# Kernel optimization log

Hardware: AMD Instinct MI355X
Metric: run time of the kernel (lower is better)

Reference implementation:

```python
import jax, jax.numpy as jnp
import numpy as np

HIDDEN = 1024
HEADS = 16
KNN = 20
EDGE_DICT = 64


def setup_inputs() -> dict:
    key = jax.random.key(0)
    ks = jax.random.split(key, 16)
    B, S, L = 2, 2000, 100
    w = lambda k, shp: jax.random.normal(k, shp, dtype=jnp.float32) * 0.02
    return {
        "c_mask": jax.random.randint(ks[0], (L,), 0, 2),
        "degrees_vec": jax.random.randint(ks[1], (L,), 0, EDGE_DICT),
        "q": jax.random.normal(ks[2], (B, S, HIDDEN), dtype=jnp.float32),
        "k": jax.random.normal(ks[3], (B, S, HIDDEN), dtype=jnp.float32),
        "v": jax.random.normal(ks[4], (B, S, HIDDEN), dtype=jnp.float32),
        "Wq": w(ks[5], (HIDDEN, HIDDEN)), "bq": jnp.zeros((HIDDEN,), jnp.float32),
        "Wk": w(ks[6], (HIDDEN, HIDDEN)), "bk": jnp.zeros((HIDDEN,), jnp.float32),
        "Wv": w(ks[7], (HIDDEN, HIDDEN)), "bv": jnp.zeros((HIDDEN,), jnp.float32),
        "Wo": w(ks[8], (HIDDEN, HIDDEN)), "bo": jnp.zeros((HIDDEN,), jnp.float32),
        "edge_emb": w(ks[9], (EDGE_DICT, HIDDEN)),
        "mask_emb": w(ks[10], (2, HIDDEN)),
    }


def reference(c_mask, degrees_vec, q, k, v, Wq, bq, Wk, bk, Wv, bv, Wo, bo, edge_emb, mask_emb):
    B, S, _ = q.shape
    d = HIDDEN // HEADS
    scale = d ** -0.5
    # torch Linear: x @ W.T + b
    qh = (q @ Wq.T + bq).reshape(B, S, HEADS, d)
    kh = (k @ Wk.T + bk).reshape(B, S, HEADS, d)
    vh = (v @ Wv.T + bv).reshape(B, S, HEADS, d)
    scores = jnp.einsum("bqhd,bkhd->bhqk", qh * scale, kh)  # [B,H,S,S]
    # edge bias: outer product of repeated embedding lookups -> [S,S]
    de = edge_emb[jnp.repeat(degrees_vec, KNN)]  # [S, hidden]
    ce = mask_emb[jnp.repeat(c_mask, KNN)]       # [S, hidden]
    bias = de @ ce.T                              # [S, S]
    attn = jax.nn.softmax(scores + bias[None, None], axis=-1)
    out = jnp.einsum("bhqk,bkhd->bqhd", attn, vh).reshape(B, S, HIDDEN)
    return out @ Wo.T + bo
```

## Files before the change

kernel.cpp:

```cpp
#include <hip/hip_runtime.h>
#include <cstdint>
#include <cstddef>

#define HIDDEN 1024
#define HEADS  16
#define DHEAD  64
#define BB     2
#define SS     2000
#define KNNR   20
#define MM     (BB*SS)

typedef __attribute__((ext_vector_type(8)))  short short8;
typedef __attribute__((ext_vector_type(4)))  float f32x4;
typedef __attribute__((ext_vector_type(16))) float f32x16;
typedef unsigned short ushort_t;
typedef unsigned int   uint_t;
typedef __attribute__((ext_vector_type(4)))  uint_t   uintx4;
typedef __attribute__((ext_vector_type(4)))  ushort_t ushortx4;
typedef __attribute__((ext_vector_type(8)))  ushort_t ushortx8;

#define LOG2E 1.4426950408889634f

__device__ __forceinline__ ushort_t f2bf(float f) {
    union { float f; uint_t u; } v; v.f = f;
    uint_t r = (v.u + 0x7FFFu + ((v.u >> 16) & 1u)) >> 16;
    return (ushort_t)r;
}

__device__ __forceinline__ uint_t cvt_pk_bf16(float a, float b) {
    uint_t r;
    asm("v_cvt_pk_bf16_f32 %0, %1, %2" : "=v"(r) : "v"(a), "v"(b));
    return r;
}
__device__ __forceinline__ void plane_swap(uint_t& a, uint_t& b) {
    asm("v_permlane32_swap_b32 %0, %1" : "+v"(a), "+v"(b));
}

__global__ void cvt3_kernel(const float* __restrict__ a, const float* __restrict__ b,
                            const float* __restrict__ c,
                            ushort_t* __restrict__ oa, ushort_t* __restrict__ ob,
                            ushort_t* __restrict__ oc, int n)
{
    const float* src; ushort_t* dst;
    if (blockIdx.y == 0)      { src = a; dst = oa; }
    else if (blockIdx.y == 1) { src = b; dst = ob; }
    else                      { src = c; dst = oc; }
    const int stride = gridDim.x * blockDim.x * 4;
    for (int i = (blockIdx.x * blockDim.x + threadIdx.x) * 4; i < n; i += stride) {
        float4 v = *(const float4*)(src + i);
        ushortx4 o;
        o.x = f2bf(v.x); o.y = f2bf(v.y); o.z = f2bf(v.z); o.w = f2bf(v.w);
        *(ushortx4*)(dst + i) = o;
    }
}

__global__ void cvt4_kernel(const float* __restrict__ a, const float* __restrict__ b,
                            const float* __restrict__ c, const float* __restrict__ d,
                            ushort_t* __restrict__ oa, ushort_t* __restrict__ ob,
                            ushort_t* __restrict__ oc, ushort_t* __restrict__ od, int n)
{
    const float* src; ushort_t* dst;
    if (blockIdx.y == 0)      { src = a; dst = oa; }
    else if (blockIdx.y == 1) { src = b; dst = ob; }
    else if (blockIdx.y == 2) { src = c; dst = oc; }
    else                      { src = d; dst = od; }
    const int stride = gridDim.x * blockDim.x * 4;
    for (int i = (blockIdx.x * blockDim.x + threadIdx.x) * 4; i < n; i += stride) {
        float4 v = *(const float4*)(src + i);
        ushortx4 o;
        o.x = f2bf(v.x); o.y = f2bf(v.y); o.z = f2bf(v.z); o.w = f2bf(v.w);
        *(ushortx4*)(dst + i) = o;
    }
}

__global__ void bias_table_kernel(const float* __restrict__ edge_emb,
                                  const float* __restrict__ mask_emb,
                                  float* __restrict__ P)
{
    const int e = blockIdx.x >> 1;
    const int m = blockIdx.x & 1;
    const int lane = threadIdx.x;
    const float* er = edge_emb + (size_t)e * HIDDEN;
    const float* mr = mask_emb + (size_t)m * HIDDEN;
    float s = 0.f;
    for (int d = lane; d < HIDDEN; d += 64) s += er[d] * mr[d];
    #pragma unroll
    for (int off = 32; off > 0; off >>= 1) s += __shfl_down(s, off, 64);
    if (lane == 0) P[e * 2 + m] = s;
}

template<int OUT_MODE>
__device__ __forceinline__
void gemm_core(const ushort_t* __restrict__ A, const ushort_t* __restrict__ Bw,
               const float* __restrict__ bias, void* __restrict__ Cp,
               int M, int m0, int n0, float oscale,
               ushort_t* As, ushort_t* Bs)
{
    const int t = threadIdx.x, l = t & 63, w = t >> 6;
    const int wr = w >> 1, wc = w & 1;
    const int g = l >> 4, r16 = l & 15;

    f32x4 acc[4][4];
    #pragma unroll
    for (int i = 0; i < 4; ++i)
        #pragma unroll
        for (int j = 0; j < 4; ++j)
            #pragma unroll
            for (int r = 0; r < 4; ++r) acc[i][j][r] = 0.f;

    for (int k0 = 0; k0 < 1024; k0 += 32) {
        __syncthreads();
        #pragma unroll
        for (int i = 0; i < 2; ++i) {
            const int c = i * 256 + w * 64 + l;
            const int row = c >> 2, kc = c & 3;
            int ra = m0 + row; ra = ra < M ? ra : M - 1;
            const ushort_t* srcA = A + (size_t)ra * 1024 + k0 + kc * 8;
            const ushort_t* srcB = Bw + (size_t)(n0 + row) * 1024 + k0 + kc * 8;
            __builtin_amdgcn_global_load_lds(
                (const __attribute__((address_space(1))) void*)srcA,
                (__attribute__((address_space(3))) void*)&As[(i * 256 + w * 64) * 8],
                16, 0, 0);
            __builtin_amdgcn_global_load_lds(
                (const __attribute__((address_space(1))) void*)srcB,
                (__attribute__((address_space(3))) void*)&Bs[(i * 256 + w * 64) * 8],
                16, 0, 0);
        }
        __syncthreads();

        short8 af[4], bf_[4];
        #pragma unroll
        for (int m = 0; m < 4; ++m)
            af[m] = *(const short8*)&As[(wr * 64 + m * 16 + r16) * 32 + g * 8];
        #pragma unroll
        for (int n = 0; n < 4; ++n)
            bf_[n] = *(const short8*)&Bs[(wc * 64 + n * 16 + r16) * 32 + g * 8];
        #pragma unroll
        for (int m = 0; m < 4; ++m)
            #pragma unroll
            for (int n = 0; n < 4; ++n)
                acc[m][n] = __builtin_amdgcn_mfma_f32_16x16x32_bf16(af[m], bf_[n], acc[m][n], 0, 0, 0);
    }

    float bv[4];
    #pragma unroll
    for (int n = 0; n < 4; ++n) bv[n] = bias[n0 + wc * 64 + n * 16 + r16];

    #pragma unroll
    for (int m = 0; m < 4; ++m)
        #pragma unroll
        for (int n = 0; n < 4; ++n)
            #pragma unroll
            for (int r = 0; r < 4; ++r) {
                const int row = m0 + wr * 64 + m * 16 + g * 4 + r;
                const int col = n0 + wc * 64 + n * 16 + r16;
                if (row < M) {
                    if (OUT_MODE == 1) {
                        const float v = (acc[m][n][r] + bv[n]) * oscale;
                        ((ushort_t*)Cp)[(size_t)row * 1024 + col] = f2bf(v);
                    } else {
                        ((float*)Cp)[(size_t)row * 1024 + col] = acc[m][n][r] + bv[n];
                    }
                }
            }
}

__global__ __launch_bounds__(256, 2)
void qkv_gemm(const ushort_t* __restrict__ qb, const ushort_t* __restrict__ kb,
              const ushort_t* __restrict__ vb,
              const ushort_t* __restrict__ Wq, const ushort_t* __restrict__ Wk,
              const ushort_t* __restrict__ Wv,
              const float* __restrict__ bq, const float* __restrict__ bk,
              const float* __restrict__ bv,
              ushort_t* __restrict__ qh, ushort_t* __restrict__ kh,
              ushort_t* __restrict__ vh)
{
    __shared__ __align__(16) ushort_t As[128 * 32];
    __shared__ __align__(16) ushort_t Bs[128 * 32];
    const int which = blockIdx.x >> 3;
    const int n0 = (blockIdx.x & 7) * 128, m0 = blockIdx.y * 128;
    const ushort_t* A; const ushort_t* Bw; const float* bias; ushort_t* dst;
    float osc = 1.f;
    if (which == 0)      { A = qb; Bw = Wq; bias = bq; dst = qh; osc = 0.125f * LOG2E; }
    else if (which == 1) { A = kb; Bw = Wk; bias = bk; dst = kh; }
    else                 { A = vb; Bw = Wv; bias = bv; dst = vh; }
    gemm_core<1>(A, Bw, bias, dst, MM, m0, n0, osc, As, Bs);
}

__global__ __launch_bounds__(256, 2)
void wo_gemm(const ushort_t* __restrict__ ctx, const ushort_t* __restrict__ Wo,
             const float* __restrict__ bo, float* __restrict__ out)
{
    __shared__ __align__(16) ushort_t As[128 * 32];
    __shared__ __align__(16) ushort_t Bs[128 * 32];
    gemm_core<0>(ctx, Wo, bo, out, MM, blockIdx.y * 128, blockIdx.x * 128, 1.f, As, Bs);
}

__global__ __launch_bounds__(256)
void transpose_v(const ushort_t* __restrict__ vh, ushort_t* __restrict__ vhT)
{
    __shared__ __align__(16) ushort_t T[64 * 72];
    const int bh = blockIdx.y, b = bh >> 4, h = bh & 15;
    const int s0 = blockIdx.x * 64;
    const int t = threadIdx.x;
    #pragma unroll
    for (int i = 0; i < 2; ++i) {
        const int c = 2 * t + i, srow = c >> 3, d8 = c & 7;
        const int s = s0 + srow;
        uint4 val = make_uint4(0, 0, 0, 0);
        if (s < SS) val = *(const uint4*)(vh + (size_t)(b * SS + s) * 1024 + h * 64 + d8 * 8);
        *(uint4*)&T[srow * 72 + d8 * 8] = val;
    }
    __syncthreads();
    #pragma unroll
    for (int i = 0; i < 2; ++i) {
        const int c = 2 * t + i, drow = c >> 3, s8 = c & 7;
        ushortx8 tmp;
        #pragma unroll
        for (int j = 0; j < 8; ++j) tmp[j] = T[(s8 * 8 + j) * 72 + drow];
        *(ushortx8*)(vhT + (size_t)(bh * 64 + drow) * 2048 + s0 + s8 * 8) = tmp;
    }
}

__global__ __launch_bounds__(256, 2)
void attn_mfma(const ushort_t* __restrict__ qh, const ushort_t* __restrict__ kh,
               const ushort_t* __restrict__ vhT, ushort_t* __restrict__ ctx,
               const int* __restrict__ c_mask, const int* __restrict__ degrees,
               const float* __restrict__ P)
{
    __shared__ __align__(16) ushort_t Ks[128 * 72];
    __shared__ __align__(16) ushort_t Vt[64 * 136];
    __shared__ uint_t kmask[64];
    __shared__ float dnm[4][32];

    const int t = threadIdx.x, l = t & 63, w = t >> 6;
    const int lo = l & 31, hi = l >> 5;
    const int bh = blockIdx.y, b = bh >> 4, h = bh & 15;
    const int qw = blockIdx.x * 128 + w * 32;

    if (t < 64) {
        uint_t m = 0;
        #pragma unroll
        for (int j = 0; j < 32; ++j) {
            int idx = (t * 32 + j) / 20; idx = idx < 100 ? idx : 99;
            m |= (uint_t)(c_mask[idx] & 1) << j;
        }
        kmask[t] = m;
    }

    int qr = qw + lo; qr = qr < SS ? qr : SS - 1;
    short8 qf[4];
    {
        const ushort_t* qp = qh + (size_t)(b * SS + qr) * 1024 + h * 64 + hi * 8;
        #pragma unroll
        for (int ks = 0; ks < 4; ++ks) qf[ks] = *(const short8*)(qp + ks * 16);
    }
    const int dv = degrees[qr / KNNR];
    const float db = (P[dv * 2 + 1] - P[dv * 2 + 0]) * LOG2E;

    float denom = 0.f;
    f32x16 accO[2];
    #pragma unroll
    for (int n = 0; n < 2; ++n)
        #pragma unroll
        for (int i = 0; i < 16; ++i) accO[n][i] = 0.f;

    uint4 kreg[4], vreg[4];
    #pragma unroll
    for (int i = 0; i < 4; ++i) {
        const int c = i * 256 + t;
        int s = c >> 3; s = s < SS ? s : SS - 1;
        kreg[i] = *(const uint4*)(kh + (size_t)(b * SS + s) * 1024 + h * 64 + (c & 7) * 8);
        vreg[i] = *(const uint4*)(vhT + (size_t)(bh * 64 + (c >> 4)) * 2048 + (c & 15) * 8);
    }

    for (int kt = 0; kt < 16; ++kt) {
        const int kt0 = kt * 128;
        __syncthreads();
        #pragma unroll
        for (int i = 0; i < 4; ++i) {
            const int c = i * 256 + t;
            *(uint4*)&Ks[(c >> 3) * 72 + (c & 7) * 8] = kreg[i];
            *(uint4*)&Vt[(c >> 4) * 136 + (c & 15) * 8] = vreg[i];
        }
        if (kt < 15) {
            const int nb = kt0 + 128;
            #pragma unroll
            for (int i = 0; i < 4; ++i) {
                const int c = i * 256 + t;
                int s = nb + (c >> 3); s = s < SS ? s : SS - 1;
                kreg[i] = *(const uint4*)(kh + (size_t)(b * SS + s) * 1024 + h * 64 + (c & 7) * 8);
                vreg[i] = *(const uint4*)(vhT + (size_t)(bh * 64 + (c >> 4)) * 2048 + nb + (c & 15) * 8);
            }
        }
        __syncthreads();

        #pragma unroll
        for (int half = 0; half < 2; ++half) {
            const int kb0 = kt0 + half * 64;

            f32x16 sc[2];
            #pragma unroll
            for (int n = 0; n < 2; ++n)
                #pragma unroll
                for (int i = 0; i < 16; ++i) sc[n][i] = 0.f;
            #pragma unroll
            for (int ks = 0; ks < 4; ++ks)
                #pragma unroll
                for (int n = 0; n < 2; ++n) {
                    const short8 kf = *(const short8*)
                        &Ks[(half * 64 + n * 32 + lo) * 72 + ks * 16 + hi * 8];
                    sc[n] = __builtin_amdgcn_mfma_f32_32x32x16_bf16(kf, qf[ks], sc[n], 0, 0, 0);
                }

            short8 pa[4];
            #pragma unroll
            for (int n = 0; n < 2; ++n) {
                const uint_t word = kmask[(kb0 + n * 32) >> 5];
                #pragma unroll
                for (int r = 0; r < 16; ++r) {
                    const int koff = (r & 3) + 8 * (r >> 2) + 4 * hi;
                    const int kcol = kb0 + n * 32 + koff;
                    const float s = sc[n][r] + (((word >> koff) & 1u) ? db : 0.f);
                    float e = exp2f(s);
                    e = (kcol < SS) ? e : 0.f;
                    denom += e;
                    sc[n][r] = e;
                }
                uint_t w0 = cvt_pk_bf16(sc[n][0], sc[n][1]);
                uint_t w2 = cvt_pk_bf16(sc[n][4], sc[n][5]);
                plane_swap(w0, w2);
                uint_t w1 = cvt_pk_bf16(sc[n][2], sc[n][3]);
                uint_t w3 = cvt_pk_bf16(sc[n][6], sc[n][7]);
                plane_swap(w1, w3);
                uint_t u0 = cvt_pk_bf16(sc[n][8],  sc[n][9]);
                uint_t u2 = cvt_pk_bf16(sc[n][12], sc[n][13]);
                plane_swap(u0, u2);
                uint_t u1 = cvt_pk_bf16(sc[n][10], sc[n][11]);
                uint_t u3 = cvt_pk_bf16(sc[n][14], sc[n][15]);
                plane_swap(u1, u3);
                uintx4 pk0, pk1;
                pk0.x = w0; pk0.y = w1; pk0.z = w2; pk0.w = w3;
                pk1.x = u0; pk1.y = u1; pk1.z = u2; pk1.w = u3;
                pa[2 * n]     = __builtin_bit_cast(short8, pk0);
                pa[2 * n + 1] = __builtin_bit_cast(short8, pk1);
            }

            #pragma unroll
            for (int ksp = 0; ksp < 4; ++ksp)
                #pragma unroll
                for (int no = 0; no < 2; ++no) {
                    const short8 vf = *(const short8*)
                        &Vt[(no * 32 + lo) * 136 + half * 64 + ksp * 16 + hi * 8];
                    accO[no] = __builtin_amdgcn_mfma_f32_32x32x16_bf16(pa[ksp], vf, accO[no], 0, 0, 0);
                }
        }
    }

    denom += __shfl_xor(denom, 32);
    if (hi == 0) dnm[w][lo] = denom;
    __syncthreads();

    #pragma unroll
    for (int r = 0; r < 16; ++r) {
        const int rp = (r & 3) + 8 * (r >> 2) + 4 * hi;
        const int q = qw + rp;
        if (q < SS) {
            const float inv = 1.f / dnm[w][rp];
            #pragma unroll
            for (int n = 0; n < 2; ++n)
                ctx[(size_t)(b * SS + q) * 1024 + h * 64 + n * 32 + lo] =
                    f2bf(accO[n][r] * inv);
        }
    }
}

extern "C" void kernel_launch(void* const* d_in, const int* in_sizes, int n_in,
                              void* d_out, int out_size, void* d_ws, size_t ws_size,
                              hipStream_t stream)
{
    const int*   c_mask   = (const int*)  d_in[0];
    const int*   degrees  = (const int*)  d_in[1];
    const float* q        = (const float*)d_in[2];
    const float* k        = (const float*)d_in[3];
    const float* v        = (const float*)d_in[4];
    const float* Wq       = (const float*)d_in[5];
    const float* bq       = (const float*)d_in[6];
    const float* Wk       = (const float*)d_in[7];
    const float* bk       = (const float*)d_in[8];
    const float* Wv       = (const float*)d_in[9];
    const float* bv       = (const float*)d_in[10];
    const float* Wo       = (const float*)d_in[11];
    const float* bo       = (const float*)d_in[12];
    const float* edge_emb = (const float*)d_in[13];
    const float* mask_emb = (const float*)d_in[14];
    float* out = (float*)d_out;

    char* ws = (char*)d_ws;
    const size_t MiB = 1024 * 1024;
    ushort_t* qb   = (ushort_t*)(ws + 0 * MiB);
    ushort_t* kb_  = (ushort_t*)(ws + 8 * MiB);
    ushort_t* vb_  = (ushort_t*)(ws + 16 * MiB);
    ushort_t* Wqb  = (ushort_t*)(ws + 24 * MiB);
    ushort_t* Wkb  = (ushort_t*)(ws + 26 * MiB);
    ushort_t* Wvb  = (ushort_t*)(ws + 28 * MiB);
    ushort_t* Wob  = (ushort_t*)(ws + 30 * MiB);
    ushort_t* qhB  = (ushort_t*)(ws + 32 * MiB);
    ushort_t* khB  = (ushort_t*)(ws + 40 * MiB);
    ushort_t* vhB  = (ushort_t*)(ws + 48 * MiB);
    float*    P    = (float*)   (ws + 56 * MiB);
    ushort_t* vhT  = kb_;
    ushort_t* ctx  = qb;

    cvt3_kernel<<<dim3(1024, 3), 256, 0, stream>>>(q, k, v, qb, kb_, vb_, MM * HIDDEN);
    cvt4_kernel<<<dim3(1024, 4), 256, 0, stream>>>(Wq, Wk, Wv, Wo, Wqb, Wkb, Wvb, Wob,
                                                   HIDDEN * HIDDEN);
    bias_table_kernel<<<dim3(128), dim3(64), 0, stream>>>(edge_emb, mask_emb, P);

    qkv_gemm<<<dim3(24, 32), 256, 0, stream>>>(qb, kb_, vb_, Wqb, Wkb, Wvb,
                                               bq, bk, bv, qhB, khB, vhB);

    transpose_v<<<dim3(32, 32), 256, 0, stream>>>(vhB, vhT);

    attn_mfma<<<dim3(16, 32), 256, 0, stream>>>(qhB, khB, vhT, ctx, c_mask, degrees, P);

    wo_gemm<<<dim3(8, 32), 256, 0, stream>>>(ctx, Wob, bo, out);
}
```

Baseline: 336.2 us.

## Double-buffer attention K/V tiles via direct global-to-LDS loads with XOR swizzle

```diff
diff --git a/kernel.cpp b/kernel.cpp
--- a/kernel.cpp
+++ b/kernel.cpp
@@ -20,6 +20,8 @@
 typedef __attribute__((ext_vector_type(8)))  ushort_t ushortx8;
 
 #define LOG2E 1.4426950408889634f
+#define AS1 __attribute__((address_space(1)))
+#define AS3 __attribute__((address_space(3)))
 
 __device__ __forceinline__ ushort_t f2bf(float f) {
     union { float f; uint_t u; } v; v.f = f;
@@ -118,12 +120,10 @@
             const ushort_t* srcA = A + (size_t)ra * 1024 + k0 + kc * 8;
             const ushort_t* srcB = Bw + (size_t)(n0 + row) * 1024 + k0 + kc * 8;
             __builtin_amdgcn_global_load_lds(
-                (const __attribute__((address_space(1))) void*)srcA,
-                (__attribute__((address_space(3))) void*)&As[(i * 256 + w * 64) * 8],
+                (const AS1 void*)srcA, (AS3 void*)&As[(i * 256 + w * 64) * 8],
                 16, 0, 0);
             __builtin_amdgcn_global_load_lds(
-                (const __attribute__((address_space(1))) void*)srcB,
-                (__attribute__((address_space(3))) void*)&Bs[(i * 256 + w * 64) * 8],
+                (const AS1 void*)srcB, (AS3 void*)&Bs[(i * 256 + w * 64) * 8],
                 16, 0, 0);
         }
         __syncthreads();
@@ -228,8 +228,8 @@
                const int* __restrict__ c_mask, const int* __restrict__ degrees,
                const float* __restrict__ P)
 {
-    __shared__ __align__(16) ushort_t Ks[128 * 72];
-    __shared__ __align__(16) ushort_t Vt[64 * 136];
+    __shared__ __align__(16) ushort_t KsB[2][128 * 64];
+    __shared__ __align__(16) ushort_t VtB[2][64 * 128];
     __shared__ uint_t kmask[64];
     __shared__ float dnm[4][32];
 
@@ -237,6 +237,7 @@
     const int lo = l & 31, hi = l >> 5;
     const int bh = blockIdx.y, b = bh >> 4, h = bh & 15;
     const int qw = blockIdx.x * 128 + w * 32;
+    const int sw = lo & 7;
 
     if (t < 64) {
         uint_t m = 0;
@@ -265,35 +266,37 @@
         #pragma unroll
         for (int i = 0; i < 16; ++i) accO[n][i] = 0.f;
 
-    uint4 kreg[4], vreg[4];
-    #pragma unroll
-    for (int i = 0; i < 4; ++i) {
-        const int c = i * 256 + t;
-        int s = c >> 3; s = s < SS ? s : SS - 1;
-        kreg[i] = *(const uint4*)(kh + (size_t)(b * SS + s) * 1024 + h * 64 + (c & 7) * 8);
-        vreg[i] = *(const uint4*)(vhT + (size_t)(bh * 64 + (c >> 4)) * 2048 + (c & 15) * 8);
-    }
-
+    auto stage = [&](int kt0, int buf) {
+        #pragma unroll
+        for (int i = 0; i < 4; ++i) {
+            const int c = i * 256 + w * 64 + l;
+            const int row = c >> 3, slot = c & 7;
+            int s = kt0 + row; s = s < SS ? s : SS - 1;
+            const int gs = slot ^ (row & 7);
+            const ushort_t* src = kh + (size_t)(b * SS + s) * 1024 + h * 64 + gs * 8;
+            __builtin_amdgcn_global_load_lds(
+                (const AS1 void*)src, (AS3 void*)&KsB[buf][(i * 256 + w * 64) * 8],
+                16, 0, 0);
+        }
+        #pragma unroll
+        for (int i = 0; i < 4; ++i) {
+            const int c = i * 256 + w * 64 + l;
+            const int d = c >> 4, slot = c & 15;
+            const int gs = (slot & 8) | ((slot ^ (d & 7)) & 7);
+            const ushort_t* src = vhT + (size_t)(bh * 64 + d) * 2048 + kt0 + gs * 8;
+            __builtin_amdgcn_global_load_lds(
+                (const AS1 void*)src, (AS3 void*)&VtB[buf][(i * 256 + w * 64) * 8],
+                16, 0, 0);
+        }
+    };
+
+    stage(0, 0);
+    __syncthreads();
+
+    int cur = 0;
     for (int kt = 0; kt < 16; ++kt) {
         const int kt0 = kt * 128;
-        __syncthreads();
-        #pragma unroll
-        for (int i = 0; i < 4; ++i) {
-            const int c = i * 256 + t;
-            *(uint4*)&Ks[(c >> 3) * 72 + (c & 7) * 8] = kreg[i];
-            *(uint4*)&Vt[(c >> 4) * 136 + (c & 15) * 8] = vreg[i];
-        }
-        if (kt < 15) {
-            const int nb = kt0 + 128;
-            #pragma unroll
-            for (int i = 0; i < 4; ++i) {
-                const int c = i * 256 + t;
-                int s = nb + (c >> 3); s = s < SS ? s : SS - 1;
-                kreg[i] = *(const uint4*)(kh + (size_t)(b * SS + s) * 1024 + h * 64 + (c & 7) * 8);
-                vreg[i] = *(const uint4*)(vhT + (size_t)(bh * 64 + (c >> 4)) * 2048 + nb + (c & 15) * 8);
-            }
-        }
-        __syncthreads();
+        if (kt < 15) stage(kt0 + 128, cur ^ 1);
 
         #pragma unroll
         for (int half = 0; half < 2; ++half) {
@@ -308,8 +311,9 @@
             for (int ks = 0; ks < 4; ++ks)
                 #pragma unroll
                 for (int n = 0; n < 2; ++n) {
+                    const int row = half * 64 + n * 32 + lo;
                     const short8 kf = *(const short8*)
-                        &Ks[(half * 64 + n * 32 + lo) * 72 + ks * 16 + hi * 8];
+                        &KsB[cur][row * 64 + ((ks * 2 + hi) ^ sw) * 8];
                     sc[n] = __builtin_amdgcn_mfma_f32_32x32x16_bf16(kf, qf[ks], sc[n], 0, 0, 0);
                 }
 
@@ -350,11 +354,15 @@
             for (int ksp = 0; ksp < 4; ++ksp)
                 #pragma unroll
                 for (int no = 0; no < 2; ++no) {
+                    const int d = no * 32 + lo;
                     const short8 vf = *(const short8*)
-                        &Vt[(no * 32 + lo) * 136 + half * 64 + ksp * 16 + hi * 8];
+                        &VtB[cur][d * 128 + (half * 8 + ((ksp * 2 + hi) ^ sw)) * 8];
                     accO[no] = __builtin_amdgcn_mfma_f32_32x32x16_bf16(pa[ksp], vf, accO[no], 0, 0, 0);
                 }
         }
+
+        __syncthreads();
+        cur ^= 1;
     }
 
     denom += __shfl_xor(denom, 32);
```

Result: faster. 278.1 us (-17.3%).
